# Kernel tuning notes

Hardware: AMD Instinct MI355X
Metric: run time of the kernel (lower is better)

## Reference

```python
import jax, jax.numpy as jnp
import numpy as np

N = 500_000   # nodes
E = 16_000_000  # edges (avg degree 32)


def setup_inputs() -> dict:
    key = jax.random.key(0)
    ks = jax.random.split(key, 12)
    x = jax.random.normal(ks[0], (N, 1), dtype=jnp.float32)
    edge_index = jax.random.randint(ks[1], (2, E), 0, N, dtype=jnp.int32)
    # GCNConv weights: conv1(1->4), conv2(4->4), conv3(4->2), classifier Linear(2->1)
    def w(k, fin, fout):
        return jax.random.normal(k, (fin, fout), dtype=jnp.float32) / np.sqrt(fin)
    W1, b1 = w(ks[2], 1, 4), jnp.zeros((4,), jnp.float32)
    W2, b2 = w(ks[3], 4, 4), jnp.zeros((4,), jnp.float32)
    W3, b3 = w(ks[4], 4, 2), jnp.zeros((2,), jnp.float32)
    Wc, bc = w(ks[5], 2, 1), jnp.zeros((1,), jnp.float32)
    return {"x": x, "edge_index": edge_index, "W1": W1, "b1": b1,
            "W2": W2, "b2": b2, "W3": W3, "b3": b3, "Wc": Wc, "bc": bc}


def _gcn_conv(h, src, dst, dinv, W, b):
    # PyG GCNConv: out = D^{-1/2}(A+I)D^{-1/2} (h W) + b
    h = h @ W  # [N, Fout], tiny Fout so transform-first is cheapest
    norm = dinv[src] * dinv[dst]          # [E]
    msg = h[src] * norm[:, None]          # [E, Fout]
    agg = jax.ops.segment_sum(msg, dst, num_segments=N)
    # self-loop contribution: norm = dinv[i]^2
    agg = agg + h * (dinv * dinv)[:, None]
    return agg + b


def reference(x, edge_index, W1, b1, W2, b2, W3, b3, Wc, bc):
    src, dst = edge_index[0], edge_index[1]
    # degree including self-loop (count of incoming edges at dst, PyG gcn_norm)
    deg = jax.ops.segment_sum(jnp.ones((E,), jnp.float32), dst, num_segments=N) + 1.0
    dinv = jax.lax.rsqrt(deg)
    h = jnp.tanh(_gcn_conv(x, src, dst, dinv, W1, b1))
    h = jnp.tanh(_gcn_conv(h, src, dst, dinv, W2, b2))
    h = jnp.tanh(_gcn_conv(h, src, dst, dinv, W3, b3))
    out = h @ Wc + bc
    return (out, h)
```

## Files before the change

kernel.cpp:

```cpp
#include <hip/hip_runtime.h>

#define NN   500000
#define NE   16000000
#define NBIN 1954

#define NBUCK   245
#define NWGA    1000
#define CHUNKA4 4000
#define NWGB    2000
#define CHUNKB4 2000
#define CAP     14336

typedef int      vint4   __attribute__((ext_vector_type(4)));
typedef float    vfloat4 __attribute__((ext_vector_type(4)));
typedef float    vfloat2 __attribute__((ext_vector_type(2)));
typedef _Float16 vhalf4  __attribute__((ext_vector_type(4)));
typedef _Float16 vhalf2  __attribute__((ext_vector_type(2)));

__global__ __launch_bounds__(256) void hist_kernel(const int* __restrict__ dst,
                                                   int* __restrict__ wgHist,
                                                   int shift, int nbin, int chunk4) {
    __shared__ int hist[NBIN];
    for (int i = threadIdx.x; i < nbin; i += 256) hist[i] = 0;
    __syncthreads();
    const vint4* d4 = (const vint4*)(dst + (size_t)blockIdx.x * chunk4 * 4);
    for (int i = threadIdx.x; i < chunk4; i += 256) {
        vint4 d = __builtin_nontemporal_load(d4 + i);
        atomicAdd(&hist[d.x >> shift], 1);
        atomicAdd(&hist[d.y >> shift], 1);
        atomicAdd(&hist[d.z >> shift], 1);
        atomicAdd(&hist[d.w >> shift], 1);
    }
    __syncthreads();
    int* row = wgHist + (size_t)blockIdx.x * nbin;
    for (int i = threadIdx.x; i < nbin; i += 256) row[i] = hist[i];
}

__global__ __launch_bounds__(256) void scanbins_kernel(int* __restrict__ wgHist,
                                                       int* __restrict__ binTotal,
                                                       int nwg, int nbin) {
    __shared__ int partials[256];
    int bin = blockIdx.x;
    int t = threadIdx.x;
    int per = (nwg + 255) / 256;
    int w0 = t * per;
    int w1 = w0 + per; if (w1 > nwg) w1 = nwg;
    int s = 0;
    for (int w = w0; w < w1; ++w) s += wgHist[(size_t)w * nbin + bin];
    partials[t] = s;
    __syncthreads();
    if (t == 0) {
        int run = 0;
        for (int i = 0; i < 256; ++i) { int tmp = partials[i]; partials[i] = run; run += tmp; }
        binTotal[bin] = run;
    }
    __syncthreads();
    int off = partials[t];
    for (int w = w0; w < w1; ++w) {
        size_t idx = (size_t)w * nbin + bin;
        int v = wgHist[idx];
        wgHist[idx] = off;
        off += v;
    }
}

__global__ void scantotal_kernel(const int* __restrict__ binTotal, int* __restrict__ binStart,
                                 int nbin) {
    __shared__ int partials[512];
    int t = threadIdx.x;
    int base = t * 4;
    int v[4]; int s = 0;
#pragma unroll
    for (int j = 0; j < 4; ++j) {
        int b = base + j;
        v[j] = (b < nbin) ? binTotal[b] : 0;
        s += v[j];
    }
    partials[t] = s;
    __syncthreads();
    if (t == 0) {
        int run = 0;
        for (int i = 0; i < 512; ++i) { int tmp = partials[i]; partials[i] = run; run += tmp; }
        binStart[nbin] = run;
    }
    __syncthreads();
    int off = partials[t];
#pragma unroll
    for (int j = 0; j < 4; ++j) {
        int b = base + j;
        if (b < nbin) binStart[b] = off;
        off += v[j];
    }
}

__global__ __launch_bounds__(256) void reorder_kernel(const int* __restrict__ src,
                                                      const int* __restrict__ dst,
                                                      const int* __restrict__ wgHist,
                                                      const int* __restrict__ binStart,
                                                      int* __restrict__ outbuf,
                                                      int shift, int nbin, int chunk4) {
    __shared__ int cur[NBIN];
    const int* row = wgHist + (size_t)blockIdx.x * nbin;
    for (int i = threadIdx.x; i < nbin; i += 256) cur[i] = binStart[i] + row[i];
    __syncthreads();
    const int mask = (1 << shift) - 1;
    const vint4* s4 = (const vint4*)(src + (size_t)blockIdx.x * chunk4 * 4);
    const vint4* d4 = (const vint4*)(dst + (size_t)blockIdx.x * chunk4 * 4);
    for (int i = threadIdx.x; i < chunk4; i += 256) {
        vint4 s = __builtin_nontemporal_load(s4 + i);
        vint4 d = __builtin_nontemporal_load(d4 + i);
        int ss[4] = {s.x, s.y, s.z, s.w};
        int dd[4] = {d.x, d.y, d.z, d.w};
#pragma unroll
        for (int k = 0; k < 4; ++k) {
            int pos = atomicAdd(&cur[dd[k] >> shift], 1);
            outbuf[pos] = (ss[k] << shift) | (dd[k] & mask);
        }
    }
}

__global__ __launch_bounds__(512) void csr_kernel(const int* __restrict__ bktStart,
                                                  const int* __restrict__ bucketbuf,
                                                  int* __restrict__ edgebuf,
                                                  const float* __restrict__ x,
                                                  float* __restrict__ dinv,
                                                  float* __restrict__ p1,
                                                  int* __restrict__ rowStart) {
    __shared__ int cnt[2048];
    __shared__ int pref[2048];
    __shared__ int partials[512];
    int b = blockIdx.x, t = threadIdx.x;
    for (int k = t; k < 2048; k += 512) cnt[k] = 0;
    __syncthreads();
    int e0 = bktStart[b], e1 = bktStart[b + 1];
    for (int i = e0 + t; i < e1; i += 512)
        atomicAdd(&cnt[bucketbuf[i] & 2047], 1);
    __syncthreads();
    int base = t * 4;
    int c0 = cnt[base], c1 = cnt[base + 1], c2 = cnt[base + 2], c3 = cnt[base + 3];
    partials[t] = c0 + c1 + c2 + c3;
    __syncthreads();
    if (t == 0) {
        int run = 0;
        for (int i = 0; i < 512; ++i) { int tmp = partials[i]; partials[i] = run; run += tmp; }
    }
    __syncthreads();
    int off = partials[t];
    int cc[4] = {c0, c1, c2, c3};
#pragma unroll
    for (int j = 0; j < 4; ++j) { pref[base + j] = off; off += cc[j]; }
#pragma unroll
    for (int j = 0; j < 4; ++j) {
        int k = base + j;
        int node = b * 2048 + k;
        if (node < NN) {
            rowStart[node] = e0 + pref[k];
            float di = rsqrtf((float)cc[j] + 1.0f);
            dinv[node] = di;
            p1[node] = x[node] * di;
        }
    }
    if (b == NBUCK - 1 && t == 0) rowStart[NN] = e1;
    __syncthreads();
#pragma unroll
    for (int j = 0; j < 4; ++j) { int k = base + j; cnt[k] = e0 + pref[k]; }
    __syncthreads();
    for (int p = 0; p < 4; ++p) {
        for (int i = e0 + t; i < e1; i += 512) {
            int e = bucketbuf[i];
            int node = e & 2047;
            if ((node >> 9) == p) {
                int pos = atomicAdd(&cnt[node], 1);
                edgebuf[pos] = e >> 11;
            }
        }
        __syncthreads();
    }
}

__global__ __launch_bounds__(256) void sortbin_kernel(const int* __restrict__ binStart,
                                                      int* __restrict__ edgebuf,
                                                      const float* __restrict__ x,
                                                      float* __restrict__ dinv,
                                                      float* __restrict__ p1,
                                                      int* __restrict__ rowStart) {
    __shared__ int stage[CAP];
    __shared__ int cnt[256];
    __shared__ int pref[256];
    __shared__ int cur[256];
    int b = blockIdx.x, t = threadIdx.x;
    cnt[t] = 0;
    __syncthreads();
    int e0 = binStart[b], e1 = binStart[b + 1];
    int n = e1 - e0;
    if (n > CAP) n = CAP;
    for (int i = t; i < n; i += 256) {
        int e = edgebuf[e0 + i];
        stage[i] = e;
        atomicAdd(&cnt[e & 255], 1);
    }
    __syncthreads();
    if (t == 0) {
        int run = 0;
        for (int i = 0; i < 256; ++i) { pref[i] = run; run += cnt[i]; }
    }
    __syncthreads();
    cur[t] = pref[t];
    int node = b * 256 + t;
    if (node < NN) {
        rowStart[node] = e0 + pref[t];
        float di = rsqrtf((float)cnt[t] + 1.0f);
        dinv[node] = di;
        p1[node] = x[node] * di;
    }
    if (b == NBIN - 1 && t == 0) rowStart[NN] = binStart[NBIN];
    __syncthreads();
    for (int i = t; i < n; i += 256) {
        int e = stage[i];
        int pos = e0 + atomicAdd(&cur[e & 255], 1);
        edgebuf[pos] = e >> 8;
    }
}

__global__ __launch_bounds__(256) void agg1_kernel(const int* __restrict__ rowStart,
                                                   const int* __restrict__ edgebuf,
                                                   const float* __restrict__ p1,
                                                   const float* __restrict__ dinv,
                                                   const float* __restrict__ W1,
                                                   const float* __restrict__ b1,
                                                   const float* __restrict__ W2,
                                                   vhalf4* __restrict__ p2h) {
    int node = blockIdx.x * blockDim.x + threadIdx.x;
    if (node >= NN) return;
    int r0 = rowStart[node], r1 = rowStart[node + 1];
    float s0 = 0.f, s1 = 0.f, s2 = 0.f, s3 = 0.f;
    float s4 = 0.f, s5 = 0.f, s6 = 0.f, s7 = 0.f;
    int k = r0;
    for (; k + 8 <= r1; k += 8) {
        int a = edgebuf[k],     b = edgebuf[k + 1];
        int c = edgebuf[k + 2], d = edgebuf[k + 3];
        int e = edgebuf[k + 4], f = edgebuf[k + 5];
        int g = edgebuf[k + 6], h = edgebuf[k + 7];
        s0 += p1[a]; s1 += p1[b]; s2 += p1[c]; s3 += p1[d];
        s4 += p1[e]; s5 += p1[f]; s6 += p1[g]; s7 += p1[h];
    }
    for (; k < r1; ++k) s0 += p1[edgebuf[k]];
    float acc = ((s0 + s1) + (s2 + s3)) + ((s4 + s5) + (s6 + s7));
    float di = dinv[node];
    float t = di * (acc + p1[node]);
    float h1[4];
#pragma unroll
    for (int f2 = 0; f2 < 4; ++f2) h1[f2] = tanhf(t * W1[f2] + b1[f2]);
    vhalf4 g;
    g.x = (_Float16)(di * (h1[0]*W2[0] + h1[1]*W2[4] + h1[2]*W2[8]  + h1[3]*W2[12]));
    g.y = (_Float16)(di * (h1[0]*W2[1] + h1[1]*W2[5] + h1[2]*W2[9]  + h1[3]*W2[13]));
    g.z = (_Float16)(di * (h1[0]*W2[2] + h1[1]*W2[6] + h1[2]*W2[10] + h1[3]*W2[14]));
    g.w = (_Float16)(di * (h1[0]*W2[3] + h1[1]*W2[7] + h1[2]*W2[11] + h1[3]*W2[15]));
    p2h[node] = g;
}

__global__ __launch_bounds__(256) void agg2_kernel(const int* __restrict__ rowStart,
                                                   const int* __restrict__ edgebuf,
                                                   const vhalf4* __restrict__ p2h,
                                                   const float* __restrict__ dinv,
                                                   const float* __restrict__ b2,
                                                   const float* __restrict__ W3,
                                                   vhalf2* __restrict__ p3h) {
    int node = blockIdx.x * blockDim.x + threadIdx.x;
    if (node >= NN) return;
    int r0 = rowStart[node], r1 = rowStart[node + 1];
    vfloat4 sA = {0.f, 0.f, 0.f, 0.f};
    vfloat4 sB = {0.f, 0.f, 0.f, 0.f};
    vfloat4 sC = {0.f, 0.f, 0.f, 0.f};
    vfloat4 sD = {0.f, 0.f, 0.f, 0.f};
    int k = r0;
    for (; k + 8 <= r1; k += 8) {
        int a = edgebuf[k],     b = edgebuf[k + 1];
        int c = edgebuf[k + 2], d = edgebuf[k + 3];
        int e = edgebuf[k + 4], f = edgebuf[k + 5];
        int g = edgebuf[k + 6], h = edgebuf[k + 7];
        vhalf4 qa = p2h[a], qb = p2h[b], qc = p2h[c], qd = p2h[d];
        vhalf4 qe = p2h[e], qf = p2h[f], qg = p2h[g], qh = p2h[h];
        sA.x += (float)qa.x + (float)qb.x; sB.x += (float)qc.x + (float)qd.x;
        sA.y += (float)qa.y + (float)qb.y; sB.y += (float)qc.y + (float)qd.y;
        sA.z += (float)qa.z + (float)qb.z; sB.z += (float)qc.z + (float)qd.z;
        sA.w += (float)qa.w + (float)qb.w; sB.w += (float)qc.w + (float)qd.w;
        sC.x += (float)qe.x + (float)qf.x; sD.x += (float)qg.x + (float)qh.x;
        sC.y += (float)qe.y + (float)qf.y; sD.y += (float)qg.y + (float)qh.y;
        sC.z += (float)qe.z + (float)qf.z; sD.z += (float)qg.z + (float)qh.z;
        sC.w += (float)qe.w + (float)qf.w; sD.w += (float)qg.w + (float)qh.w;
    }
    for (; k < r1; ++k) {
        vhalf4 q = p2h[edgebuf[k]];
        sA.x += (float)q.x; sA.y += (float)q.y; sA.z += (float)q.z; sA.w += (float)q.w;
    }
    float di = dinv[node];
    vhalf4 pw = p2h[node];
    float h2[4];
    h2[0] = tanhf(di * (sA.x + sB.x + sC.x + sD.x + (float)pw.x) + b2[0]);
    h2[1] = tanhf(di * (sA.y + sB.y + sC.y + sD.y + (float)pw.y) + b2[1]);
    h2[2] = tanhf(di * (sA.z + sB.z + sC.z + sD.z + (float)pw.z) + b2[2]);
    h2[3] = tanhf(di * (sA.w + sB.w + sC.w + sD.w + (float)pw.w) + b2[3]);
    vhalf2 o;
    o.x = (_Float16)(di * (h2[0]*W3[0] + h2[1]*W3[2] + h2[2]*W3[4] + h2[3]*W3[6]));
    o.y = (_Float16)(di * (h2[0]*W3[1] + h2[1]*W3[3] + h2[2]*W3[5] + h2[3]*W3[7]));
    p3h[node] = o;
}

__global__ __launch_bounds__(256) void agg3_kernel(const int* __restrict__ rowStart,
                                                   const int* __restrict__ edgebuf,
                                                   const vhalf2* __restrict__ p3h,
                                                   const float* __restrict__ dinv,
                                                   const float* __restrict__ b3,
                                                   const float* __restrict__ Wc,
                                                   const float* __restrict__ bc,
                                                   float* __restrict__ out) {
    int node = blockIdx.x * blockDim.x + threadIdx.x;
    if (node >= NN) return;
    int r0 = rowStart[node], r1 = rowStart[node + 1];
    float ax = 0.f, ay = 0.f, bx = 0.f, by = 0.f;
    float cx = 0.f, cy = 0.f, dx = 0.f, dy = 0.f;
    int k = r0;
    for (; k + 8 <= r1; k += 8) {
        int a = edgebuf[k],     b = edgebuf[k + 1];
        int c = edgebuf[k + 2], d = edgebuf[k + 3];
        int e = edgebuf[k + 4], f = edgebuf[k + 5];
        int g = edgebuf[k + 6], h = edgebuf[k + 7];
        vhalf2 qa = p3h[a], qb = p3h[b], qc = p3h[c], qd = p3h[d];
        vhalf2 qe = p3h[e], qf = p3h[f], qg = p3h[g], qh = p3h[h];
        ax += (float)qa.x + (float)qb.x; bx += (float)qc.x + (float)qd.x;
        ay += (float)qa.y + (float)qb.y; by += (float)qc.y + (float)qd.y;
        cx += (float)qe.x + (float)qf.x; dx += (float)qg.x + (float)qh.x;
        cy += (float)qe.y + (float)qf.y; dy += (float)qg.y + (float)qh.y;
    }
    for (; k < r1; ++k) {
        vhalf2 q = p3h[edgebuf[k]];
        ax += (float)q.x; ay += (float)q.y;
    }
    float di = dinv[node];
    vhalf2 pw = p3h[node];
    float h0 = tanhf(di * (ax + bx + cx + dx + (float)pw.x) + b3[0]);
    float h1 = tanhf(di * (ay + by + cy + dy + (float)pw.y) + b3[1]);
    __builtin_nontemporal_store(h0 * Wc[0] + h1 * Wc[1] + bc[0], out + node);
    vfloat2 hh; hh.x = h0; hh.y = h1;
    __builtin_nontemporal_store(hh, (vfloat2*)(out + NN) + node);
}


extern "C" void kernel_launch(void* const* d_in, const int* in_sizes, int n_in,
                              void* d_out, int out_size, void* d_ws, size_t ws_size,
                              hipStream_t stream) {
    const float* x   = (const float*)d_in[0];
    const int*   ei  = (const int*)d_in[1];
    const float* W1  = (const float*)d_in[2];
    const float* b1  = (const float*)d_in[3];
    const float* W2  = (const float*)d_in[4];
    const float* b2  = (const float*)d_in[5];
    const float* W3  = (const float*)d_in[6];
    const float* b3  = (const float*)d_in[7];
    const float* Wc  = (const float*)d_in[8];
    const float* bc  = (const float*)d_in[9];
    float* out = (float*)d_out;
    float* ws  = (float*)d_ws;

    const int* src = ei;
    const int* dst = ei + NE;

    float*  dinv     = ws;
    float*  p1       = ws + (size_t)NN;
    vhalf4* p2h      = (vhalf4*)(ws + 2ull * NN);
    vhalf2* p3h      = (vhalf2*)(ws + 4ull * NN);
    int*    rowStart = (int*)(ws + 5ull * NN);
    int*    tail     = (int*)(ws + 6ull * NN + 1);

    const int B = 256;
    const int aggGrid = (NN + B - 1) / B;

    const size_t needA = (6ull * NN + 1 + (size_t)NWGA * NBUCK + NBUCK + NBUCK + 1
                          + 2ull * NE) * 4ull;

    if (ws_size >= needA) {
        int* wgHist    = tail;
        int* bktTotal  = wgHist + (size_t)NWGA * NBUCK;
        int* bktStart  = bktTotal + NBUCK;
        int* bucketbuf = bktStart + NBUCK + 1;
        int* edgebuf   = bucketbuf + (size_t)NE;

        hipLaunchKernelGGL(hist_kernel, dim3(NWGA), dim3(B), 0, stream,
                           dst, wgHist, 11, NBUCK, CHUNKA4);
        hipLaunchKernelGGL(scanbins_kernel, dim3(NBUCK), dim3(B), 0, stream,
                           wgHist, bktTotal, NWGA, NBUCK);
        hipLaunchKernelGGL(scantotal_kernel, dim3(1), dim3(512), 0, stream,
                           bktTotal, bktStart, NBUCK);
        hipLaunchKernelGGL(reorder_kernel, dim3(NWGA), dim3(B), 0, stream,
                           src, dst, wgHist, bktStart, bucketbuf, 11, NBUCK, CHUNKA4);
        hipLaunchKernelGGL(csr_kernel, dim3(NBUCK), dim3(512), 0, stream,
                           bktStart, bucketbuf, edgebuf, x, dinv, p1, rowStart);
        hipLaunchKernelGGL(agg1_kernel, dim3(aggGrid), dim3(B), 0, stream,
                           rowStart, edgebuf, p1, dinv, W1, b1, W2, p2h);
        hipLaunchKernelGGL(agg2_kernel, dim3(aggGrid), dim3(B), 0, stream,
                           rowStart, edgebuf, p2h, dinv, b2, W3, p3h);
        hipLaunchKernelGGL(agg3_kernel, dim3(aggGrid), dim3(B), 0, stream,
                           rowStart, edgebuf, p3h, dinv, b3, Wc, bc, out);
    } else {
        int* wgHist   = tail;
        int* binTotal = wgHist + (size_t)NWGB * NBIN;
        int* binStart = binTotal + NBIN;
        int* edgebuf  = binStart + NBIN + 1;

        hipLaunchKernelGGL(hist_kernel, dim3(NWGB), dim3(B), 0, stream,
                           dst, wgHist, 8, NBIN, CHUNKB4);
        hipLaunchKernelGGL(scanbins_kernel, dim3(NBIN), dim3(B), 0, stream,
                           wgHist, binTotal, NWGB, NBIN);
        hipLaunchKernelGGL(scantotal_kernel, dim3(1), dim3(512), 0, stream,
                           binTotal, binStart, NBIN);
        hipLaunchKernelGGL(reorder_kernel, dim3(NWGB), dim3(B), 0, stream,
                           src, dst, wgHist, binStart, edgebuf, 8, NBIN, CHUNKB4);
        hipLaunchKernelGGL(sortbin_kernel, dim3(NBIN), dim3(B), 0, stream,
                           binStart, edgebuf, x, dinv, p1, rowStart);
        hipLaunchKernelGGL(agg1_kernel, dim3(aggGrid), dim3(B), 0, stream,
                           rowStart, edgebuf, p1, dinv, W1, b1, W2, p2h);
        hipLaunchKernelGGL(agg2_kernel, dim3(aggGrid), dim3(B), 0, stream,
                           rowStart, edgebuf, p2h, dinv, b2, W3, p3h);
        hipLaunchKernelGGL(agg3_kernel, dim3(aggGrid), dim3(B), 0, stream,
                           rowStart, edgebuf, p3h, dinv, b3, Wc, bc, out);
    }
}
```

Measured before the change: 762.6 us.

## Split CSR build into count kernel and 4x-parallel scatter kernel

The single csr_kernel, which counted per-node degrees and then scattered edges in four serial passes per bucket, is split into two kernels. count_kernel computes degrees, rowStart, dinv and p1 using an unrolled nontemporal count loop. scat_kernel launches four workgroups per bucket, each handling one 512-node quarter, so the four scatter passes run in parallel across more CUs. The cost is an extra launch, and each bucket's edge list is now read four times by separate workgroups instead of sequentially by one.

```diff
diff --git a/kernel.cpp b/kernel.cpp
--- a/kernel.cpp
+++ b/kernel.cpp
@@ -119,22 +119,31 @@
     }
 }
 
-__global__ __launch_bounds__(512) void csr_kernel(const int* __restrict__ bktStart,
-                                                  const int* __restrict__ bucketbuf,
-                                                  int* __restrict__ edgebuf,
-                                                  const float* __restrict__ x,
-                                                  float* __restrict__ dinv,
-                                                  float* __restrict__ p1,
-                                                  int* __restrict__ rowStart) {
+__global__ __launch_bounds__(512) void count_kernel(const int* __restrict__ bktStart,
+                                                    const int* __restrict__ bucketbuf,
+                                                    const float* __restrict__ x,
+                                                    float* __restrict__ dinv,
+                                                    float* __restrict__ p1,
+                                                    int* __restrict__ rowStart) {
     __shared__ int cnt[2048];
-    __shared__ int pref[2048];
     __shared__ int partials[512];
     int b = blockIdx.x, t = threadIdx.x;
     for (int k = t; k < 2048; k += 512) cnt[k] = 0;
     __syncthreads();
     int e0 = bktStart[b], e1 = bktStart[b + 1];
-    for (int i = e0 + t; i < e1; i += 512)
-        atomicAdd(&cnt[bucketbuf[i] & 2047], 1);
+    int i = e0 + t;
+    for (; i + 3 * 512 < e1; i += 4 * 512) {
+        int a = __builtin_nontemporal_load(bucketbuf + i);
+        int c = __builtin_nontemporal_load(bucketbuf + i + 512);
+        int d = __builtin_nontemporal_load(bucketbuf + i + 1024);
+        int e = __builtin_nontemporal_load(bucketbuf + i + 1536);
+        atomicAdd(&cnt[a & 2047], 1);
+        atomicAdd(&cnt[c & 2047], 1);
+        atomicAdd(&cnt[d & 2047], 1);
+        atomicAdd(&cnt[e & 2047], 1);
+    }
+    for (; i < e1; i += 512)
+        atomicAdd(&cnt[__builtin_nontemporal_load(bucketbuf + i) & 2047], 1);
     __syncthreads();
     int base = t * 4;
     int c0 = cnt[base], c1 = cnt[base + 1], c2 = cnt[base + 2], c3 = cnt[base + 3];
@@ -142,39 +151,44 @@
     __syncthreads();
     if (t == 0) {
         int run = 0;
-        for (int i = 0; i < 512; ++i) { int tmp = partials[i]; partials[i] = run; run += tmp; }
+        for (int k = 0; k < 512; ++k) { int tmp = partials[k]; partials[k] = run; run += tmp; }
     }
     __syncthreads();
     int off = partials[t];
     int cc[4] = {c0, c1, c2, c3};
-#pragma unroll
-    for (int j = 0; j < 4; ++j) { pref[base + j] = off; off += cc[j]; }
 #pragma unroll
     for (int j = 0; j < 4; ++j) {
         int k = base + j;
         int node = b * 2048 + k;
         if (node < NN) {
-            rowStart[node] = e0 + pref[k];
+            rowStart[node] = e0 + off;
             float di = rsqrtf((float)cc[j] + 1.0f);
             dinv[node] = di;
             p1[node] = x[node] * di;
         }
+        off += cc[j];
     }
     if (b == NBUCK - 1 && t == 0) rowStart[NN] = e1;
-    __syncthreads();
-#pragma unroll
-    for (int j = 0; j < 4; ++j) { int k = base + j; cnt[k] = e0 + pref[k]; }
-    __syncthreads();
-    for (int p = 0; p < 4; ++p) {
-        for (int i = e0 + t; i < e1; i += 512) {
-            int e = bucketbuf[i];
-            int node = e & 2047;
-            if ((node >> 9) == p) {
-                int pos = atomicAdd(&cnt[node], 1);
-                edgebuf[pos] = e >> 11;
-            }
+}
+
+__global__ __launch_bounds__(512) void scat_kernel(const int* __restrict__ bktStart,
+                                                   const int* __restrict__ bucketbuf,
+                                                   const int* __restrict__ rowStart,
+                                                   int* __restrict__ edgebuf) {
+    __shared__ int cur[512];
+    int b = blockIdx.x >> 2, p = blockIdx.x & 3;
+    int t = threadIdx.x;
+    int node = b * 2048 + p * 512 + t;
+    cur[t] = (node <= NN) ? rowStart[node] : 0;
+    __syncthreads();
+    int e0 = bktStart[b], e1 = bktStart[b + 1];
+    for (int i = e0 + t; i < e1; i += 512) {
+        int e = __builtin_nontemporal_load(bucketbuf + i);
+        int loc = e & 2047;
+        if ((loc >> 9) == p) {
+            int pos = atomicAdd(&cur[loc & 511], 1);
+            edgebuf[pos] = e >> 11;
         }
-        __syncthreads();
     }
 }
 
@@ -394,8 +408,10 @@
                            bktTotal, bktStart, NBUCK);
         hipLaunchKernelGGL(reorder_kernel, dim3(NWGA), dim3(B), 0, stream,
                            src, dst, wgHist, bktStart, bucketbuf, 11, NBUCK, CHUNKA4);
-        hipLaunchKernelGGL(csr_kernel, dim3(NBUCK), dim3(512), 0, stream,
-                           bktStart, bucketbuf, edgebuf, x, dinv, p1, rowStart);
+        hipLaunchKernelGGL(count_kernel, dim3(NBUCK), dim3(512), 0, stream,
+                           bktStart, bucketbuf, x, dinv, p1, rowStart);
+        hipLaunchKernelGGL(scat_kernel, dim3(NBUCK * 4), dim3(512), 0, stream,
+                           bktStart, bucketbuf, rowStart, edgebuf);
         hipLaunchKernelGGL(agg1_kernel, dim3(aggGrid), dim3(B), 0, stream,
                            rowStart, edgebuf, p1, dinv, W1, b1, W2, p2h);
         hipLaunchKernelGGL(agg2_kernel, dim3(aggGrid), dim3(B), 0, stream,
```

Measured after the change: 925.2 us. +21.3%, slower.
